# Optimization experiments

Measured on AMD Instinct MI355X. Metric: run time of the kernel, lower is better.

The kernel has to match this reference:

```python
import jax, jax.numpy as jnp
import numpy as np

SMU_ALPHA = 0.25
SMU_MU = 1.0e6  # repo's act.SMU default: large mu -> smooth leaky-relu (max(x, alpha*x))

def smu(x):
    a = SMU_ALPHA
    return 0.5 * ((1.0 + a) * x + (1.0 - a) * x * jax.lax.erf(SMU_MU * (1.0 - a) * x))

def setup_inputs() -> dict:
    key = jax.random.key(0)
    ks = jax.random.split(key, 6)
    B, N, D = 8, 4096, 1024
    xavier = float(np.sqrt(6.0 / (D + D)))
    def lin_w(k):
        return jax.random.uniform(k, (D, D), jnp.float32, -xavier, xavier)
    return {
        "x": jax.random.normal(ks[0], (B, N, D), jnp.float32),
        "Wvr": lin_w(ks[1]), "bvr": jnp.zeros((D,), jnp.float32),
        "Wvi": lin_w(ks[2]), "bvi": jnp.zeros((D,), jnp.float32),
        "Wk": lin_w(ks[3]), "bk": jnp.zeros((D,), jnp.float32),
        "Wq": lin_w(ks[4]), "bq": jnp.zeros((D,), jnp.float32),
    }

def reference(x, Wvr, bvr, Wvi, bvi, Wk, bk, Wq, bq):
    # real input: real and imag branches both see x
    value_real = jnp.einsum('bnd,ed->bne', x, Wvr) + bvr
    value_imag = jnp.einsum('bnd,ed->bne', x, Wvi) + bvi
    # GLU: v_real * tanh(softplus(v_imag)); dropout disabled (p=0)
    value = value_real * jnp.tanh(jax.nn.softplus(value_imag))
    key_ = jnp.einsum('bnd,ed->bne', x, Wk) + bk
    query = jnp.einsum('bnd,ed->bne', x, Wq) + bq
    # L2 normalize along the sequence dim (dim=1)
    key_n = key_ / (jnp.linalg.norm(key_, axis=1, keepdims=True) + 1e-5)
    query_n = query / (jnp.linalg.norm(query, axis=1, keepdims=True) + 1e-5)
    feature_attn = smu(jnp.einsum('bnd,bne->bde', key_n, query_n))  # [B, D, D]
    return jnp.einsum('bnd,bde->bne', value, feature_attn)
```

## Files before the change

### kernel.cpp

```cpp
#include <hip/hip_runtime.h>
#include <math.h>

typedef __bf16 bf16x8 __attribute__((ext_vector_type(8)));
typedef float f32x4 __attribute__((ext_vector_type(4)));

#define MTOT 32768
#define DD   1024
#define NSEQ 4096
#define BB   8

__device__ __forceinline__ void async16(const void* gp, void* lp) {
  __builtin_amdgcn_global_load_lds(
      (__attribute__((address_space(1))) void*)(const_cast<void*>(gp)),
      (__attribute__((address_space(3))) void*)(lp), 16, 0, 0);
}

__device__ __forceinline__ unsigned short f2bf(float f) {
  union { float f; unsigned int u; } v; v.f = f;
  unsigned int r = v.u + 0x7fffu + ((v.u >> 16) & 1u);
  return (unsigned short)(r >> 16);
}
__device__ __forceinline__ float bf2f(unsigned short u) {
  union { unsigned int u; float f; } v; v.u = ((unsigned int)u) << 16; return v.f;
}
__device__ __forceinline__ unsigned pk2(float a, float b) {
  return (unsigned)f2bf(a) | ((unsigned)f2bf(b) << 16);
}

__device__ __forceinline__ unsigned lds_off(void* p) {
  return (unsigned)(unsigned long long)
      (__attribute__((address_space(3))) void*)p;
}
#define DSRI(dst, base, off) \
  asm volatile("ds_read_b128 %0, %1 offset:" #off : "=v"(dst) : "v"(base))

#define MFMA_ __builtin_amdgcn_mfma_f32_16x16x32_bf16

__global__ void cvt_bf16(const float* __restrict__ in, unsigned short* __restrict__ out, int n) {
  int i = (blockIdx.x * blockDim.x + threadIdx.x) * 8;
  if (i >= n) return;
  float4 a = *(const float4*)(in + i);
  float4 b = *(const float4*)(in + i + 4);
  ushort4 o0, o1;
  o0.x = f2bf(a.x); o0.y = f2bf(a.y); o0.z = f2bf(a.z); o0.w = f2bf(a.w);
  o1.x = f2bf(b.x); o1.y = f2bf(b.y); o1.z = f2bf(b.z); o1.w = f2bf(b.w);
  *(ushort4*)(out + i) = o0;
  *(ushort4*)(out + i + 4) = o1;
}

__global__ void cvt_w(const float* __restrict__ w0, const float* __restrict__ w1,
                      const float* __restrict__ w2, const float* __restrict__ w3,
                      unsigned short* __restrict__ out) {
  int z = blockIdx.y;
  const float* in = (z == 0) ? w0 : (z == 1) ? w1 : (z == 2) ? w2 : w3;
  int i = (blockIdx.x * blockDim.x + threadIdx.x) * 8;
  float4 a = *(const float4*)(in + i);
  float4 b = *(const float4*)(in + i + 4);
  ushort4 o0, o1;
  o0.x = f2bf(a.x); o0.y = f2bf(a.y); o0.z = f2bf(a.z); o0.w = f2bf(a.w);
  o1.x = f2bf(b.x); o1.y = f2bf(b.y); o1.z = f2bf(b.z); o1.w = f2bf(b.w);
  unsigned short* o = out + (size_t)z * DD * DD;
  *(ushort4*)(o + i) = o0;
  *(ushort4*)(o + i + 4) = o1;
}

template<int LDG>
__device__ __forceinline__ void stage_half(const unsigned short* __restrict__ g,
                                           int row0, int k0,
                                           unsigned short* lds, int tid) {
#pragma unroll
  for (int l = 0; l < 2; ++l) {
    int u = l * 512 + tid;
    int r = u >> 3;
    int sl = (u & 7) ^ (r & 7);
    async16(g + (size_t)(row0 + r) * LDG + k0 + sl * 8, (char*)lds + u * 16);
  }
}

__global__ __launch_bounds__(512, 2) void proj_all(
    const unsigned short* __restrict__ xb,
    const unsigned short* __restrict__ Wb,
    const float* __restrict__ bvr, const float* __restrict__ bvi,
    const float* __restrict__ bk,  const float* __restrict__ bq,
    unsigned short* __restrict__ oV,
    unsigned short* __restrict__ Kt,  unsigned short* __restrict__ Qt,
    float* __restrict__ rnacc) {
  __shared__ __align__(16) unsigned short smem[65536];

  const int bx = blockIdx.x;
  const int swz = (bx & 7) * 64 + (bx >> 3);
  const int m0 = (swz >> 2) * 256;
  const int n0 = (swz & 3) * 256;
  const int z = blockIdx.z;

  const int tid = threadIdx.x;
  const int w = tid >> 6, lane = tid & 63;
  const int wr = w >> 2, wc = w & 3;
  const int lq = lane >> 4, lr = lane & 15;
  const int sx = lr & 7;
  const int arow0 = wr * 128 + lr;
  const int brow0 = wc * 64 + lr;

  f32x4 acc[8][4];
#pragma unroll
  for (int i = 0; i < 8; i++)
#pragma unroll
    for (int j = 0; j < 4; j++) acc[i][j] = (f32x4)(0.f);

  unsigned pkx[8][4], pky[8][4];

  const int NT = 16;

  const unsigned sbase = lds_off(smem);
  const unsigned sw0 = (unsigned)((lq ^ sx) << 4);
  const unsigned sw1 = (unsigned)(((4 | lq) ^ sx) << 4);
  unsigned aA0 = sbase + arow0 * 128 + sw0;
  unsigned aA1 = sbase + arow0 * 128 + sw1;
  unsigned aB0 = sbase + 32768 + brow0 * 128 + sw0;
  unsigned aB1 = sbase + 32768 + brow0 * 128 + sw1;

  const int npass = (z == 0) ? 2 : 1;
  for (int pass = 0; pass < npass; ++pass) {
    const unsigned short* W =
        (z == 0) ? (Wb + (size_t)(pass == 0 ? 1 : 0) * DD * DD)
                 : (Wb + (size_t)(z + 1) * DD * DD);

    stage_half<1024>(xb, m0,       0,  smem,                     tid);
    stage_half<1024>(xb, m0 + 128, 0,  smem + 8192,              tid);
    stage_half<1024>(W,  n0,       0,  smem + 16384,             tid);
    stage_half<1024>(W,  n0 + 128, 0,  smem + 16384 + 8192,      tid);
    stage_half<1024>(W,  n0,       64, smem + 32768 + 16384,     tid);
    stage_half<1024>(W,  n0 + 128, 64, smem + 32768 + 16384 + 8192, tid);
    asm volatile("s_waitcnt vmcnt(4)" ::: "memory");
    __builtin_amdgcn_s_barrier();

    for (int t = 0; t < NT; ++t) {
      bf16x8 bfr[4][2], aL[4][2];
      DSRI(aL[0][0], aA0, 0);    DSRI(aL[0][1], aA1, 0);
      DSRI(bfr[0][0], aB0, 0);    DSRI(bfr[0][1], aB1, 0);
      DSRI(bfr[1][0], aB0, 2048); DSRI(bfr[1][1], aB1, 2048);
      DSRI(bfr[2][0], aB0, 4096); DSRI(bfr[2][1], aB1, 4096);
      DSRI(bfr[3][0], aB0, 6144); DSRI(bfr[3][1], aB1, 6144);
      DSRI(aL[1][0], aA0, 2048); DSRI(aL[1][1], aA1, 2048);
      DSRI(aL[2][0], aA0, 4096); DSRI(aL[2][1], aA1, 4096);
      DSRI(aL[3][0], aA0, 6144); DSRI(aL[3][1], aA1, 6144);
      if (t + 1 < NT) {
        stage_half<1024>(xb, m0,       (t + 1) * 64, smem + ((t + 1) & 1) * 32768, tid);
        stage_half<1024>(xb, m0 + 128, (t + 1) * 64, smem + ((t + 1) & 1) * 32768 + 8192, tid);
      }
      __builtin_amdgcn_s_barrier();
      asm volatile("s_waitcnt lgkmcnt(6)" ::: "memory");
      __builtin_amdgcn_sched_barrier(0);
      __builtin_amdgcn_s_setprio(1);
#pragma unroll
      for (int nj = 0; nj < 4; ++nj) {
        acc[0][nj] = MFMA_(aL[0][0], bfr[nj][0], acc[0][nj], 0, 0, 0);
        acc[0][nj] = MFMA_(aL[0][1], bfr[nj][1], acc[0][nj], 0, 0, 0);
      }
      asm volatile("s_waitcnt lgkmcnt(0)" ::: "memory");
      __builtin_amdgcn_sched_barrier(0);
#pragma unroll
      for (int mi = 1; mi < 4; ++mi)
#pragma unroll
        for (int nj = 0; nj < 4; ++nj) {
          acc[mi][nj] = MFMA_(aL[mi][0], bfr[nj][0], acc[mi][nj], 0, 0, 0);
          acc[mi][nj] = MFMA_(aL[mi][1], bfr[nj][1], acc[mi][nj], 0, 0, 0);
        }
      __builtin_amdgcn_s_setprio(0);
      __builtin_amdgcn_sched_barrier(0);
      __builtin_amdgcn_s_barrier();

      bf16x8 aH[4][2];
      DSRI(aH[0][0], aA0, 8192);  DSRI(aH[0][1], aA1, 8192);
      DSRI(aH[1][0], aA0, 10240); DSRI(aH[1][1], aA1, 10240);
      DSRI(aH[2][0], aA0, 12288); DSRI(aH[2][1], aA1, 12288);
      DSRI(aH[3][0], aA0, 14336); DSRI(aH[3][1], aA1, 14336);
      if (t + 2 < NT) {
        stage_half<1024>(W, n0,       (t + 2) * 64, smem + (t & 1) * 32768 + 16384, tid);
        stage_half<1024>(W, n0 + 128, (t + 2) * 64, smem + (t & 1) * 32768 + 16384 + 8192, tid);
      }
      __builtin_amdgcn_s_barrier();
      asm volatile("s_waitcnt lgkmcnt(4)" ::: "memory");
      __builtin_amdgcn_sched_barrier(0);
      __builtin_amdgcn_s_setprio(1);
#pragma unroll
      for (int mi = 0; mi < 2; ++mi)
#pragma unroll
        for (int nj = 0; nj < 4; ++nj) {
          acc[4 + mi][nj] = MFMA_(aH[mi][0], bfr[nj][0], acc[4 + mi][nj], 0, 0, 0);
          acc[4 + mi][nj] = MFMA_(aH[mi][1], bfr[nj][1], acc[4 + mi][nj], 0, 0, 0);
        }
      asm volatile("s_waitcnt lgkmcnt(0)" ::: "memory");
      __builtin_amdgcn_sched_barrier(0);
#pragma unroll
      for (int mi = 2; mi < 4; ++mi)
#pragma unroll
        for (int nj = 0; nj < 4; ++nj) {
          acc[4 + mi][nj] = MFMA_(aH[mi][0], bfr[nj][0], acc[4 + mi][nj], 0, 0, 0);
          acc[4 + mi][nj] = MFMA_(aH[mi][1], bfr[nj][1], acc[4 + mi][nj], 0, 0, 0);
        }
      __builtin_amdgcn_s_setprio(0);
      __builtin_amdgcn_sched_barrier(0);
      if (t < NT - 2)       asm volatile("s_waitcnt vmcnt(4)" ::: "memory");
      else if (t == NT - 2) asm volatile("s_waitcnt vmcnt(0)" ::: "memory");
      __builtin_amdgcn_s_barrier();

      aA0 ^= 65536u; aA1 ^= 65536u; aB0 ^= 65536u; aB1 ^= 65536u;
    }

    if (z == 0 && pass == 0) {
#pragma unroll
      for (int nj = 0; nj < 4; ++nj) {
        int col = n0 + wc * 64 + nj * 16 + lr;
        float bv = bvi[col];
#pragma unroll
        for (int mrep = 0; mrep < 8; ++mrep) {
          pkx[mrep][nj] = pk2(acc[mrep][nj][0] + bv, acc[mrep][nj][1] + bv);
          pky[mrep][nj] = pk2(acc[mrep][nj][2] + bv, acc[mrep][nj][3] + bv);
          acc[mrep][nj] = (f32x4)(0.f);
        }
      }
    }
  }

  if (z == 0) {
#pragma unroll
    for (int nj = 0; nj < 4; ++nj) {
      int col = n0 + wc * 64 + nj * 16 + lr;
      float bv = bvr[col];
#pragma unroll
      for (int mrep = 0; mrep < 8; ++mrep) {
        int rowb = m0 + wr * 128 + mrep * 16 + lq * 4;
#pragma unroll
        for (int r = 0; r < 4; ++r) {
          float vr = bf2f(f2bf(acc[mrep][nj][r] + bv));
          unsigned p = (r < 2) ? pkx[mrep][nj] : pky[mrep][nj];
          float vi = bf2f((unsigned short)((r & 1) ? (p >> 16) : (p & 0xffffu)));
          float g;
          if (vi > 10.f) g = 1.f;
          else { float tt = __expf(vi); float u = tt * (tt + 2.f); g = u / (u + 2.f); }
          oV[(size_t)(rowb + r) * DD + col] = f2bf(vr * g);
        }
      }
    }
  } else {
    const float* bias = (z == 1) ? bk : bq;
    unsigned short* outp = (z == 1) ? Kt : Qt;
    const int which = z - 1;
    const int b = m0 >> 12;
    const int nbase = m0 & 4095;
    float* racc = rnacc + which * (BB * DD) + b * DD;
    unsigned short* T = smem;
    const int SP2 = 264;
#pragma unroll
    for (int ch = 0; ch < 2; ++ch) {
      if ((wc >> 1) == ch) {
#pragma unroll
        for (int nj = 0; nj < 4; ++nj) {
          int cloc = (wc & 1) * 64 + nj * 16 + lr;
          float bv = bias[n0 + ch * 128 + cloc];
#pragma unroll
          for (int mrep = 0; mrep < 8; ++mrep) {
            int rowb = wr * 128 + mrep * 16 + lq * 4;
            ushort4 pk;
            pk.x = f2bf(acc[mrep][nj][0] + bv); pk.y = f2bf(acc[mrep][nj][1] + bv);
            pk.z = f2bf(acc[mrep][nj][2] + bv); pk.w = f2bf(acc[mrep][nj][3] + bv);
            *(ushort4*)(T + cloc * SP2 + rowb) = pk;
          }
        }
      }
      __syncthreads();
#pragma unroll
      for (int p = 0; p < 8; ++p) {
        int dl = p * 16 + (tid >> 5);
        int nc = (tid & 31) * 8;
        ushort4 v0 = *(const ushort4*)(T + dl * SP2 + nc);
        ushort4 v1 = *(const ushort4*)(T + dl * SP2 + nc + 4);
        int d = n0 + ch * 128 + dl;
        *(ushort4*)(outp + (size_t)(b * DD + d) * NSEQ + nbase + nc)     = v0;
        *(ushort4*)(outp + (size_t)(b * DD + d) * NSEQ + nbase + nc + 4) = v1;
        float s = bf2f(v0.x)*bf2f(v0.x) + bf2f(v0.y)*bf2f(v0.y) + bf2f(v0.z)*bf2f(v0.z) + bf2f(v0.w)*bf2f(v0.w)
                + bf2f(v1.x)*bf2f(v1.x) + bf2f(v1.y)*bf2f(v1.y) + bf2f(v1.z)*bf2f(v1.z) + bf2f(v1.w)*bf2f(v1.w);
#pragma unroll
        for (int off = 1; off < 32; off <<= 1) s += __shfl_xor(s, off, 32);
        if ((tid & 31) == 0) atomicAdd(&racc[d], s);
      }
      __syncthreads();
    }
  }
}

__global__ void finalize_rn(float* __restrict__ rn) {
  int i = blockIdx.x * blockDim.x + threadIdx.x;
  rn[i] = 1.f / (sqrtf(rn[i]) + 1e-5f);
}

__global__ __launch_bounds__(512, 2) void attn_gemm(
    const unsigned short* __restrict__ Qt, const unsigned short* __restrict__ Kt,
    const float* __restrict__ rn, unsigned short* __restrict__ fat) {
  __shared__ __align__(16) unsigned short smem[57344];

  const int b = blockIdx.z;
  const int d0 = blockIdx.x * 128;
  const int e0 = blockIdx.y * 256;
  const unsigned short* A  = Qt + (size_t)b * DD * NSEQ;
  const unsigned short* Bm = Kt + (size_t)b * DD * NSEQ;
  unsigned short* out = fat + (size_t)b * DD * DD;

  const int tid = threadIdx.x;
  const int w = tid >> 6, lane = tid & 63;
  const int wr = w >> 1, wc = w & 1;
  const int lq = lane >> 4, lr = lane & 15;
  const int sx = lr & 7;
  const int arow0 = wr * 64 + lr;
  const int brow0 = wc * 64 + lr;

  f32x4 acc[4][4];
#pragma unroll
  for (int i = 0; i < 4; i++)
#pragma unroll
    for (int j = 0; j < 4; j++) acc[i][j] = (f32x4)(0.f);

  const int NT = 64;

  const unsigned sbase = lds_off(smem);
  const unsigned sw0 = (unsigned)((lq ^ sx) << 4);
  const unsigned sw1 = (unsigned)(((4 | lq) ^ sx) << 4);
  unsigned aA0 = sbase + arow0 * 128 + sw0;
  unsigned aA1 = sbase + arow0 * 128 + sw1;
  unsigned aB0 = sbase + 32768 + brow0 * 128 + sw0;
  unsigned aB1 = sbase + 32768 + brow0 * 128 + sw1;

  stage_half<NSEQ>(A,  e0,       0,  smem,                 tid);
  stage_half<NSEQ>(A,  e0 + 128, 0,  smem + 8192,          tid);
  stage_half<NSEQ>(Bm, d0,       0,  smem + 16384,         tid);
  stage_half<NSEQ>(Bm, d0,       64, smem + 32768 + 16384, tid);
  asm volatile("s_waitcnt vmcnt(2)" ::: "memory");
  __builtin_amdgcn_s_barrier();

  for (int t = 0; t < NT; ++t) {
    bf16x8 bfr[4][2], aL[2][2];
    DSRI(aL[0][0], aA0, 0);    DSRI(aL[0][1], aA1, 0);
    DSRI(bfr[0][0], aB0, 0);    DSRI(bfr[0][1], aB1, 0);
    DSRI(bfr[1][0], aB0, 2048); DSRI(bfr[1][1], aB1, 2048);
    DSRI(bfr[2][0], aB0, 4096); DSRI(bfr[2][1], aB1, 4096);
    DSRI(bfr[3][0], aB0, 6144); DSRI(bfr[3][1], aB1, 6144);
    DSRI(aL[1][0], aA0, 2048); DSRI(aL[1][1], aA1, 2048);
    if (t + 1 < NT) {
      stage_half<NSEQ>(A, e0,       (t + 1) * 64, smem + ((t + 1) & 1) * 32768, tid);
      stage_half<NSEQ>(A, e0 + 128, (t + 1) * 64, smem + ((t + 1) & 1) * 32768 + 8192, tid);
    }
    __builtin_amdgcn_s_barrier();
    asm volatile("s_waitcnt lgkmcnt(2)" ::: "memory");
    __builtin_amdgcn_sched_barrier(0);
    __builtin_amdgcn_s_setprio(1);
#pragma unroll
    for (int nj = 0; nj < 4; ++nj) {
      acc[0][nj] = MFMA_(aL[0][0], bfr[nj][0], acc[0][nj], 0, 0, 0);
      acc[0][nj] = MFMA_(aL[0][1], bfr[nj][1], acc[0][nj], 0, 0, 0);
    }
    asm volatile("s_waitcnt lgkmcnt(0)" ::: "memory");
    __builtin_amdgcn_sched_barrier(0);
#pragma unroll
    for (int nj = 0; nj < 4; ++nj) {
      acc[1][nj] = MFMA_(aL[1][0], bfr[nj][0], acc[1][nj], 0, 0, 0);
      acc[1][nj] = MFMA_(aL[1][1], bfr[nj][1], acc[1][nj], 0, 0, 0);
    }
    __builtin_amdgcn_s_setprio(0);
    __builtin_amdgcn_sched_barrier(0);
    __builtin_amdgcn_s_barrier();

    bf16x8 aH[2][2];
    DSRI(aH[0][0], aA0, 4096); DSRI(aH[0][1], aA1, 4096);
    DSRI(aH[1][0], aA0, 6144); DSRI(aH[1][1], aA1, 6144);
    if (t + 2 < NT) {
      stage_half<NSEQ>(Bm, d0, (t + 2) * 64, smem + (t & 1) * 32768 + 16384, tid);
    }
    __builtin_amdgcn_s_barrier();
    asm volatile("s_waitcnt lgkmcnt(2)" ::: "memory");
    __builtin_amdgcn_sched_barrier(0);
    __builtin_amdgcn_s_setprio(1);
#pragma unroll
    for (int nj = 0; nj < 4; ++nj) {
      acc[2][nj] = MFMA_(aH[0][0], bfr[nj][0], acc[2][nj], 0, 0, 0);
      acc[2][nj] = MFMA_(aH[0][1], bfr[nj][1], acc[2][nj], 0, 0, 0);
    }
    asm volatile("s_waitcnt lgkmcnt(0)" ::: "memory");
    __builtin_amdgcn_sched_barrier(0);
#pragma unroll
    for (int nj = 0; nj < 4; ++nj) {
      acc[3][nj] = MFMA_(aH[1][0], bfr[nj][0], acc[3][nj], 0, 0, 0);
      acc[3][nj] = MFMA_(aH[1][1], bfr[nj][1], acc[3][nj], 0, 0, 0);
    }
    __builtin_amdgcn_s_setprio(0);
    __builtin_amdgcn_sched_barrier(0);
    if (t < NT - 2)       asm volatile("s_waitcnt vmcnt(2)" ::: "memory");
    else if (t == NT - 2) asm volatile("s_waitcnt vmcnt(0)" ::: "memory");
    __builtin_amdgcn_s_barrier();

    aA0 ^= 65536u; aA1 ^= 65536u; aB0 ^= 65536u; aB1 ^= 65536u;
  }

#pragma unroll
  for (int nj = 0; nj < 4; ++nj) {
    int col = d0 + wc * 64 + nj * 16 + lr;
    float rk = rn[b * DD + col];
#pragma unroll
    for (int mi = 0; mi < 4; ++mi) {
      int rowb = e0 + wr * 64 + mi * 16 + lq * 4;
#pragma unroll
      for (int r = 0; r < 4; ++r) {
        float rq = rn[BB * DD + b * DD + rowb + r];
        float c = acc[mi][nj][r] * rq * rk;
        c = (c > 0.f) ? c : 0.25f * c;
        out[(size_t)(rowb + r) * DD + col] = f2bf(c);
      }
    }
  }
}

__global__ __launch_bounds__(512, 2) void out_gemm(
    const unsigned short* __restrict__ V, const unsigned short* __restrict__ fat,
    float* __restrict__ out) {
  __shared__ __align__(16) unsigned short smem[65536];

  const int bx = blockIdx.x;
  const int swz = (bx & 7) * 64 + (bx >> 3);
  const int m0 = (swz >> 2) * 256;
  const int e0 = (swz & 3) * 256;
  const int b = m0 >> 12;
  const unsigned short* Bm = fat + (size_t)b * DD * DD;

  const int tid = threadIdx.x;
  const int w = tid >> 6, lane = tid & 63;
  const int wr = w >> 2, wc = w & 3;
  const int lq = lane >> 4, lr = lane & 15;
  const int sx = lr & 7;
  const int arow0 = wr * 128 + lr;
  const int brow0 = wc * 64 + lr;

  f32x4 acc[8][4];
#pragma unroll
  for (int i = 0; i < 8; i++)
#pragma unroll
    for (int j = 0; j < 4; j++) acc[i][j] = (f32x4)(0.f);

  const int NT = 16;

  const unsigned sbase = lds_off(smem);
  const unsigned sw0 = (unsigned)((lq ^ sx) << 4);
  const unsigned sw1 = (unsigned)(((4 | lq) ^ sx) << 4);
  unsigned aA0 = sbase + arow0 * 128 + sw0;
  unsigned aA1 = sbase + arow0 * 128 + sw1;
  unsigned aB0 = sbase + 32768 + brow0 * 128 + sw0;
  unsigned aB1 = sbase + 32768 + brow0 * 128 + sw1;

  stage_half<1024>(V,  m0,       0,  smem,                        tid);
  stage_half<1024>(V,  m0 + 128, 0,  smem + 8192,                 tid);
  stage_half<1024>(Bm, e0,       0,  smem + 16384,                tid);
  stage_half<1024>(Bm, e0 + 128, 0,  smem + 16384 + 8192,         tid);
  stage_half<1024>(Bm, e0,       64, smem + 32768 + 16384,        tid);
  stage_half<1024>(Bm, e0 + 128, 64, smem + 32768 + 16384 + 8192, tid);
  asm volatile("s_waitcnt vmcnt(4)" ::: "memory");
  __builtin_amdgcn_s_barrier();

  for (int t = 0; t < NT; ++t) {
    bf16x8 bfr[4][2], aL[4][2];
    DSRI(aL[0][0], aA0, 0);    DSRI(aL[0][1], aA1, 0);
    DSRI(bfr[0][0], aB0, 0);    DSRI(bfr[0][1], aB1, 0);
    DSRI(bfr[1][0], aB0, 2048); DSRI(bfr[1][1], aB1, 2048);
    DSRI(bfr[2][0], aB0, 4096); DSRI(bfr[2][1], aB1, 4096);
    DSRI(bfr[3][0], aB0, 6144); DSRI(bfr[3][1], aB1, 6144);
    DSRI(aL[1][0], aA0, 2048); DSRI(aL[1][1], aA1, 2048);
    DSRI(aL[2][0], aA0, 4096); DSRI(aL[2][1], aA1, 4096);
    DSRI(aL[3][0], aA0, 6144); DSRI(aL[3][1], aA1, 6144);
    if (t + 1 < NT) {
      stage_half<1024>(V, m0,       (t + 1) * 64, smem + ((t + 1) & 1) * 32768, tid);
      stage_half<1024>(V, m0 + 128, (t + 1) * 64, smem + ((t + 1) & 1) * 32768 + 8192, tid);
    }
    __builtin_amdgcn_s_barrier();
    asm volatile("s_waitcnt lgkmcnt(6)" ::: "memory");
    __builtin_amdgcn_sched_barrier(0);
    __builtin_amdgcn_s_setprio(1);
#pragma unroll
    for (int nj = 0; nj < 4; ++nj) {
      acc[0][nj] = MFMA_(aL[0][0], bfr[nj][0], acc[0][nj], 0, 0, 0);
      acc[0][nj] = MFMA_(aL[0][1], bfr[nj][1], acc[0][nj], 0, 0, 0);
    }
    asm volatile("s_waitcnt lgkmcnt(0)" ::: "memory");
    __builtin_amdgcn_sched_barrier(0);
#pragma unroll
    for (int mi = 1; mi < 4; ++mi)
#pragma unroll
      for (int nj = 0; nj < 4; ++nj) {
        acc[mi][nj] = MFMA_(aL[mi][0], bfr[nj][0], acc[mi][nj], 0, 0, 0);
        acc[mi][nj] = MFMA_(aL[mi][1], bfr[nj][1], acc[mi][nj], 0, 0, 0);
      }
    __builtin_amdgcn_s_setprio(0);
    __builtin_amdgcn_sched_barrier(0);
    __builtin_amdgcn_s_barrier();

    bf16x8 aH[4][2];
    DSRI(aH[0][0], aA0, 8192);  DSRI(aH[0][1], aA1, 8192);
    DSRI(aH[1][0], aA0, 10240); DSRI(aH[1][1], aA1, 10240);
    DSRI(aH[2][0], aA0, 12288); DSRI(aH[2][1], aA1, 12288);
    DSRI(aH[3][0], aA0, 14336); DSRI(aH[3][1], aA1, 14336);
    if (t + 2 < NT) {
      stage_half<1024>(Bm, e0,       (t + 2) * 64, smem + (t & 1) * 32768 + 16384, tid);
      stage_half<1024>(Bm, e0 + 128, (t + 2) * 64, smem + (t & 1) * 32768 + 16384 + 8192, tid);
    }
    __builtin_amdgcn_s_barrier();
    asm volatile("s_waitcnt lgkmcnt(4)" ::: "memory");
    __builtin_amdgcn_sched_barrier(0);
    __builtin_amdgcn_s_setprio(1);
#pragma unroll
    for (int mi = 0; mi < 2; ++mi)
#pragma unroll
      for (int nj = 0; nj < 4; ++nj) {
        acc[4 + mi][nj] = MFMA_(aH[mi][0], bfr[nj][0], acc[4 + mi][nj], 0, 0, 0);
        acc[4 + mi][nj] = MFMA_(aH[mi][1], bfr[nj][1], acc[4 + mi][nj], 0, 0, 0);
      }
    asm volatile("s_waitcnt lgkmcnt(0)" ::: "memory");
    __builtin_amdgcn_sched_barrier(0);
#pragma unroll
    for (int mi = 2; mi < 4; ++mi)
#pragma unroll
      for (int nj = 0; nj < 4; ++nj) {
        acc[4 + mi][nj] = MFMA_(aH[mi][0], bfr[nj][0], acc[4 + mi][nj], 0, 0, 0);
        acc[4 + mi][nj] = MFMA_(aH[mi][1], bfr[nj][1], acc[4 + mi][nj], 0, 0, 0);
      }
    __builtin_amdgcn_s_setprio(0);
    __builtin_amdgcn_sched_barrier(0);
    if (t < NT - 2)       asm volatile("s_waitcnt vmcnt(4)" ::: "memory");
    else if (t == NT - 2) asm volatile("s_waitcnt vmcnt(0)" ::: "memory");
    __builtin_amdgcn_s_barrier();

    aA0 ^= 65536u; aA1 ^= 65536u; aB0 ^= 65536u; aB1 ^= 65536u;
  }

#pragma unroll
  for (int nj = 0; nj < 4; ++nj) {
    int col = e0 + wc * 64 + nj * 16 + lr;
#pragma unroll
    for (int mrep = 0; mrep < 8; ++mrep) {
      int rowb = m0 + wr * 128 + mrep * 16 + lq * 4;
#pragma unroll
      for (int r = 0; r < 4; ++r)
        out[(size_t)(rowb + r) * DD + col] = acc[mrep][nj][r];
    }
  }
}

extern "C" void kernel_launch(void* const* d_in, const int* in_sizes, int n_in,
                              void* d_out, int out_size, void* d_ws, size_t ws_size,
                              hipStream_t stream) {
  const float* x   = (const float*)d_in[0];
  const float* Wvr = (const float*)d_in[1];
  const float* bvr = (const float*)d_in[2];
  const float* Wvi = (const float*)d_in[3];
  const float* bvi = (const float*)d_in[4];
  const float* Wk  = (const float*)d_in[5];
  const float* bk  = (const float*)d_in[6];
  const float* Wq  = (const float*)d_in[7];
  const float* bq  = (const float*)d_in[8];
  float* out = (float*)d_out;

  char* p = (char*)d_ws;
  unsigned short* xb  = (unsigned short*)p; p += (size_t)MTOT * DD * 2;
  unsigned short* Wb  = (unsigned short*)p; p += 4ull * DD * DD * 2;
  unsigned short* Kt  = (unsigned short*)p; p += (size_t)BB * DD * NSEQ * 2;
  unsigned short* Qt  = (unsigned short*)p; p += (size_t)BB * DD * NSEQ * 2;
  unsigned short* Vb  = (unsigned short*)p; p += (size_t)MTOT * DD * 2;
  unsigned short* fat = (unsigned short*)p; p += (size_t)BB * DD * DD * 2;
  float* rn = (float*)p; p += 2ull * BB * DD * sizeof(float);

  int nx = MTOT * DD;
  int nw = DD * DD;
  cvt_bf16<<<nx / 8 / 256, 256, 0, stream>>>(x, xb, nx);
  cvt_w<<<dim3(nw / 8 / 256, 4), 256, 0, stream>>>(Wvr, Wvi, Wk, Wq, Wb);
  hipMemsetAsync(rn, 0, 2ull * BB * DD * sizeof(float), stream);

  proj_all<<<dim3(512, 1, 3), 512, 0, stream>>>(
      xb, Wb, bvr, bvi, bk, bq, Vb, Kt, Qt, rn);

  finalize_rn<<<2 * BB * DD / 256, 256, 0, stream>>>(rn);

  attn_gemm<<<dim3(DD / 128, DD / 256, BB), 512, 0, stream>>>(Qt, Kt, rn, fat);
  out_gemm<<<dim3(512), 512, 0, stream>>>(Vb, fat, out);
}
```

Before: 717.0 us.

## Split value projection into dedicated kernel computing real and imag GEMMs together

The fused projection kernel had z=0 blocks running two sequential GEMM passes (imag then real), which made them twice as long as the K/Q blocks and unbalanced the grid. A new proj_v kernel uses 256x128 tiles and computes both Wvr and Wvi products at once from a shared x tile, so each x load feeds two GEMMs. K/Q projection becomes its own kernel with the same tiling as before. This balances work across blocks and halves x traffic for the value branch. The cost is an extra launch, a smaller N tile per block, and more accumulator registers.

```diff
diff --git a/kernel.cpp b/kernel.cpp
--- a/kernel.cpp
+++ b/kernel.cpp
@@ -22,9 +22,6 @@
 }
 __device__ __forceinline__ float bf2f(unsigned short u) {
   union { unsigned int u; float f; } v; v.u = ((unsigned int)u) << 16; return v.f;
-}
-__device__ __forceinline__ unsigned pk2(float a, float b) {
-  return (unsigned)f2bf(a) | ((unsigned)f2bf(b) << 16);
 }
 
 __device__ __forceinline__ unsigned lds_off(void* p) {
@@ -77,12 +74,140 @@
   }
 }
 
-__global__ __launch_bounds__(512, 2) void proj_all(
+__global__ __launch_bounds__(512, 2) void proj_v(
     const unsigned short* __restrict__ xb,
     const unsigned short* __restrict__ Wb,
     const float* __restrict__ bvr, const float* __restrict__ bvi,
+    unsigned short* __restrict__ oV) {
+  __shared__ __align__(16) unsigned short smem[65536];
+
+  const int bx = blockIdx.x;
+  const int swz = (bx & 7) * 128 + (bx >> 3);
+  const int m0 = (swz >> 3) * 256;
+  const int n0 = (swz & 7) * 128;
+  const unsigned short* Wr = Wb;
+  const unsigned short* Wi = Wb + (size_t)DD * DD;
+
+  const int tid = threadIdx.x;
+  const int w = tid >> 6, lane = tid & 63;
+  const int wrow = w >> 1, wcol = w & 1;
+  const int lq = lane >> 4, lr = lane & 15;
+  const int sx = lr & 7;
+  const int arow0 = wrow * 64 + lr;
+  const int brow0 = wcol * 64 + lr;
+
+  f32x4 accr[4][4], acci[4][4];
+#pragma unroll
+  for (int i = 0; i < 4; i++)
+#pragma unroll
+    for (int j = 0; j < 4; j++) { accr[i][j] = (f32x4)(0.f); acci[i][j] = (f32x4)(0.f); }
+
+  const int NT = 16;
+
+  const unsigned sbase = lds_off(smem);
+  const unsigned sw0 = (unsigned)((lq ^ sx) << 4);
+  const unsigned sw1 = (unsigned)(((4 | lq) ^ sx) << 4);
+  unsigned aA0 = sbase + arow0 * 128 + sw0;
+  unsigned aA1 = sbase + arow0 * 128 + sw1;
+  unsigned aR0 = sbase + 32768 + brow0 * 128 + sw0;
+  unsigned aR1 = sbase + 32768 + brow0 * 128 + sw1;
+  unsigned aI0 = sbase + 49152 + brow0 * 128 + sw0;
+  unsigned aI1 = sbase + 49152 + brow0 * 128 + sw1;
+
+  stage_half<1024>(xb, m0,       0,  smem,                  tid);
+  stage_half<1024>(xb, m0 + 128, 0,  smem + 8192,           tid);
+  stage_half<1024>(Wr, n0,       0,  smem + 16384,          tid);
+  stage_half<1024>(Wi, n0,       0,  smem + 24576,          tid);
+  stage_half<1024>(Wr, n0,       64, smem + 32768 + 16384,  tid);
+  stage_half<1024>(Wi, n0,       64, smem + 32768 + 24576,  tid);
+  asm volatile("s_waitcnt vmcnt(4)" ::: "memory");
+  __builtin_amdgcn_s_barrier();
+
+  for (int t = 0; t < NT; ++t) {
+    bf16x8 aF[4][2], bR[4][2], bI[4][2];
+    DSRI(aF[0][0], aA0, 0);    DSRI(aF[0][1], aA1, 0);
+    DSRI(bR[0][0], aR0, 0);    DSRI(bR[0][1], aR1, 0);
+    DSRI(bR[1][0], aR0, 2048); DSRI(bR[1][1], aR1, 2048);
+    DSRI(bR[2][0], aR0, 4096); DSRI(bR[2][1], aR1, 4096);
+    DSRI(bR[3][0], aR0, 6144); DSRI(bR[3][1], aR1, 6144);
+    DSRI(aF[1][0], aA0, 2048); DSRI(aF[1][1], aA1, 2048);
+    DSRI(aF[2][0], aA0, 4096); DSRI(aF[2][1], aA1, 4096);
+    DSRI(aF[3][0], aA0, 6144); DSRI(aF[3][1], aA1, 6144);
+    DSRI(bI[0][0], aI0, 0);    DSRI(bI[0][1], aI1, 0);
+    DSRI(bI[1][0], aI0, 2048); DSRI(bI[1][1], aI1, 2048);
+    DSRI(bI[2][0], aI0, 4096); DSRI(bI[2][1], aI1, 4096);
+    DSRI(bI[3][0], aI0, 6144); DSRI(bI[3][1], aI1, 6144);
+    if (t + 1 < NT) {
+      stage_half<1024>(xb, m0,       (t + 1) * 64, smem + ((t + 1) & 1) * 32768, tid);
+      stage_half<1024>(xb, m0 + 128, (t + 1) * 64, smem + ((t + 1) & 1) * 32768 + 8192, tid);
+    }
+    asm volatile("s_waitcnt lgkmcnt(14)" ::: "memory");
+    __builtin_amdgcn_sched_barrier(0);
+    __builtin_amdgcn_s_setprio(1);
+#pragma unroll
+    for (int nj = 0; nj < 4; ++nj) {
+      accr[0][nj] = MFMA_(aF[0][0], bR[nj][0], accr[0][nj], 0, 0, 0);
+      accr[0][nj] = MFMA_(aF[0][1], bR[nj][1], accr[0][nj], 0, 0, 0);
+    }
+    asm volatile("s_waitcnt lgkmcnt(8)" ::: "memory");
+    __builtin_amdgcn_sched_barrier(0);
+#pragma unroll
+    for (int mi = 1; mi < 4; ++mi)
+#pragma unroll
+      for (int nj = 0; nj < 4; ++nj) {
+        accr[mi][nj] = MFMA_(aF[mi][0], bR[nj][0], accr[mi][nj], 0, 0, 0);
+        accr[mi][nj] = MFMA_(aF[mi][1], bR[nj][1], accr[mi][nj], 0, 0, 0);
+      }
+    __builtin_amdgcn_s_setprio(0);
+    asm volatile("s_waitcnt lgkmcnt(0)" ::: "memory");
+    __builtin_amdgcn_sched_barrier(0);
+    __builtin_amdgcn_s_barrier();
+    if (t + 2 < NT) {
+      stage_half<1024>(Wr, n0, (t + 2) * 64, smem + (t & 1) * 32768 + 16384, tid);
+      stage_half<1024>(Wi, n0, (t + 2) * 64, smem + (t & 1) * 32768 + 24576, tid);
+    }
+    __builtin_amdgcn_s_setprio(1);
+#pragma unroll
+    for (int mi = 0; mi < 4; ++mi)
+#pragma unroll
+      for (int nj = 0; nj < 4; ++nj) {
+        acci[mi][nj] = MFMA_(aF[mi][0], bI[nj][0], acci[mi][nj], 0, 0, 0);
+        acci[mi][nj] = MFMA_(aF[mi][1], bI[nj][1], acci[mi][nj], 0, 0, 0);
+      }
+    __builtin_amdgcn_s_setprio(0);
+    __builtin_amdgcn_sched_barrier(0);
+    if (t < NT - 2)       asm volatile("s_waitcnt vmcnt(4)" ::: "memory");
+    else if (t == NT - 2) asm volatile("s_waitcnt vmcnt(0)" ::: "memory");
+    __builtin_amdgcn_s_barrier();
+
+    aA0 ^= 65536u; aA1 ^= 65536u; aR0 ^= 65536u; aR1 ^= 65536u;
+    aI0 ^= 65536u; aI1 ^= 65536u;
+  }
+
+#pragma unroll
+  for (int nj = 0; nj < 4; ++nj) {
+    int col = n0 + wcol * 64 + nj * 16 + lr;
+    float br_ = bvr[col], bi_ = bvi[col];
+#pragma unroll
+    for (int mi = 0; mi < 4; ++mi) {
+      int rowb = m0 + wrow * 64 + mi * 16 + lq * 4;
+#pragma unroll
+      for (int r = 0; r < 4; ++r) {
+        float vr = bf2f(f2bf(accr[mi][nj][r] + br_));
+        float vi = bf2f(f2bf(acci[mi][nj][r] + bi_));
+        float g;
+        if (vi > 10.f) g = 1.f;
+        else { float tt = __expf(vi); float u = tt * (tt + 2.f); g = u / (u + 2.f); }
+        oV[(size_t)(rowb + r) * DD + col] = f2bf(vr * g);
+      }
+    }
+  }
+}
+
+__global__ __launch_bounds__(512, 2) void proj_kq(
+    const unsigned short* __restrict__ xb,
+    const unsigned short* __restrict__ Wb,
     const float* __restrict__ bk,  const float* __restrict__ bq,
-    unsigned short* __restrict__ oV,
     unsigned short* __restrict__ Kt,  unsigned short* __restrict__ Qt,
     float* __restrict__ rnacc) {
   __shared__ __align__(16) unsigned short smem[65536];
@@ -92,6 +217,8 @@
   const int m0 = (swz >> 2) * 256;
   const int n0 = (swz & 3) * 256;
   const int z = blockIdx.z;
+  const unsigned short* W = Wb + (size_t)(2 + z) * DD * DD;
+  const float* bias = (z == 0) ? bk : bq;
 
   const int tid = threadIdx.x;
   const int w = tid >> 6, lane = tid & 63;
@@ -107,8 +234,6 @@
 #pragma unroll
     for (int j = 0; j < 4; j++) acc[i][j] = (f32x4)(0.f);
 
-  unsigned pkx[8][4], pky[8][4];
-
   const int NT = 16;
 
   const unsigned sbase = lds_off(smem);
@@ -119,137 +244,94 @@
   unsigned aB0 = sbase + 32768 + brow0 * 128 + sw0;
   unsigned aB1 = sbase + 32768 + brow0 * 128 + sw1;
 
-  const int npass = (z == 0) ? 2 : 1;
-  for (int pass = 0; pass < npass; ++pass) {
-    const unsigned short* W =
-        (z == 0) ? (Wb + (size_t)(pass == 0 ? 1 : 0) * DD * DD)
-                 : (Wb + (size_t)(z + 1) * DD * DD);
-
-    stage_half<1024>(xb, m0,       0,  smem,                     tid);
-    stage_half<1024>(xb, m0 + 128, 0,  smem + 8192,              tid);
-    stage_half<1024>(W,  n0,       0,  smem + 16384,             tid);
-    stage_half<1024>(W,  n0 + 128, 0,  smem + 16384 + 8192,      tid);
-    stage_half<1024>(W,  n0,       64, smem + 32768 + 16384,     tid);
-    stage_half<1024>(W,  n0 + 128, 64, smem + 32768 + 16384 + 8192, tid);
-    asm volatile("s_waitcnt vmcnt(4)" ::: "memory");
-    __builtin_amdgcn_s_barrier();
-
-    for (int t = 0; t < NT; ++t) {
-      bf16x8 bfr[4][2], aL[4][2];
-      DSRI(aL[0][0], aA0, 0);    DSRI(aL[0][1], aA1, 0);
-      DSRI(bfr[0][0], aB0, 0);    DSRI(bfr[0][1], aB1, 0);
-      DSRI(bfr[1][0], aB0, 2048); DSRI(bfr[1][1], aB1, 2048);
-      DSRI(bfr[2][0], aB0, 4096); DSRI(bfr[2][1], aB1, 4096);
-      DSRI(bfr[3][0], aB0, 6144); DSRI(bfr[3][1], aB1, 6144);
-      DSRI(aL[1][0], aA0, 2048); DSRI(aL[1][1], aA1, 2048);
-      DSRI(aL[2][0], aA0, 4096); DSRI(aL[2][1], aA1, 4096);
-      DSRI(aL[3][0], aA0, 6144); DSRI(aL[3][1], aA1, 6144);
-      if (t + 1 < NT) {
-        stage_half<1024>(xb, m0,       (t + 1) * 64, smem + ((t + 1) & 1) * 32768, tid);
-        stage_half<1024>(xb, m0 + 128, (t + 1) * 64, smem + ((t + 1) & 1) * 32768 + 8192, tid);
-      }
-      __builtin_amdgcn_s_barrier();
-      asm volatile("s_waitcnt lgkmcnt(6)" ::: "memory");
-      __builtin_amdgcn_sched_barrier(0);
-      __builtin_amdgcn_s_setprio(1);
-#pragma unroll
-      for (int nj = 0; nj < 4; ++nj) {
-        acc[0][nj] = MFMA_(aL[0][0], bfr[nj][0], acc[0][nj], 0, 0, 0);
-        acc[0][nj] = MFMA_(aL[0][1], bfr[nj][1], acc[0][nj], 0, 0, 0);
-      }
-      asm volatile("s_waitcnt lgkmcnt(0)" ::: "memory");
-      __builtin_amdgcn_sched_barrier(0);
-#pragma unroll
-      for (int mi = 1; mi < 4; ++mi)
-#pragma unroll
-        for (int nj = 0; nj < 4; ++nj) {
-          acc[mi][nj] = MFMA_(aL[mi][0], bfr[nj][0], acc[mi][nj], 0, 0, 0);
-          acc[mi][nj] = MFMA_(aL[mi][1], bfr[nj][1], acc[mi][nj], 0, 0, 0);
-        }
-      __builtin_amdgcn_s_setprio(0);
-      __builtin_amdgcn_sched_barrier(0);
-      __builtin_amdgcn_s_barrier();
-
-      bf16x8 aH[4][2];
-      DSRI(aH[0][0], aA0, 8192);  DSRI(aH[0][1], aA1, 8192);
-      DSRI(aH[1][0], aA0, 10240); DSRI(aH[1][1], aA1, 10240);
-      DSRI(aH[2][0], aA0, 12288); DSRI(aH[2][1], aA1, 12288);
-      DSRI(aH[3][0], aA0, 14336); DSRI(aH[3][1], aA1, 14336);
-      if (t + 2 < NT) {
-        stage_half<1024>(W, n0,       (t + 2) * 64, smem + (t & 1) * 32768 + 16384, tid);
-        stage_half<1024>(W, n0 + 128, (t + 2) * 64, smem + (t & 1) * 32768 + 16384 + 8192, tid);
-      }
-      __builtin_amdgcn_s_barrier();
-      asm volatile("s_waitcnt lgkmcnt(4)" ::: "memory");
-      __builtin_amdgcn_sched_barrier(0);
-      __builtin_amdgcn_s_setprio(1);
-#pragma unroll
-      for (int mi = 0; mi < 2; ++mi)
-#pragma unroll
-        for (int nj = 0; nj < 4; ++nj) {
-          acc[4 + mi][nj] = MFMA_(aH[mi][0], bfr[nj][0], acc[4 + mi][nj], 0, 0, 0);
-          acc[4 + mi][nj] = MFMA_(aH[mi][1], bfr[nj][1], acc[4 + mi][nj], 0, 0, 0);
-        }
-      asm volatile("s_waitcnt lgkmcnt(0)" ::: "memory");
-      __builtin_amdgcn_sched_barrier(0);
-#pragma unroll
-      for (int mi = 2; mi < 4; ++mi)
-#pragma unroll
-        for (int nj = 0; nj < 4; ++nj) {
-          acc[4 + mi][nj] = MFMA_(aH[mi][0], bfr[nj][0], acc[4 + mi][nj], 0, 0, 0);
-          acc[4 + mi][nj] = MFMA_(aH[mi][1], bfr[nj][1], acc[4 + mi][nj], 0, 0, 0);
-        }
-      __builtin_amdgcn_s_setprio(0);
-      __builtin_amdgcn_sched_barrier(0);
-      if (t < NT - 2)       asm volatile("s_waitcnt vmcnt(4)" ::: "memory");
-      else if (t == NT - 2) asm volatile("s_waitcnt vmcnt(0)" ::: "memory");
-      __builtin_amdgcn_s_barrier();
-
-      aA0 ^= 65536u; aA1 ^= 65536u; aB0 ^= 65536u; aB1 ^= 65536u;
-    }
-
-    if (z == 0 && pass == 0) {
-#pragma unroll
-      for (int nj = 0; nj < 4; ++nj) {
-        int col = n0 + wc * 64 + nj * 16 + lr;
-        float bv = bvi[col];
-#pragma unroll
-        for (int mrep = 0; mrep < 8; ++mrep) {
-          pkx[mrep][nj] = pk2(acc[mrep][nj][0] + bv, acc[mrep][nj][1] + bv);
-          pky[mrep][nj] = pk2(acc[mrep][nj][2] + bv, acc[mrep][nj][3] + bv);
-          acc[mrep][nj] = (f32x4)(0.f);
-        }
-      }
-    }
-  }
-
-  if (z == 0) {
+  stage_half<1024>(xb, m0,       0,  smem,                     tid);
+  stage_half<1024>(xb, m0 + 128, 0,  smem + 8192,              tid);
+  stage_half<1024>(W,  n0,       0,  smem + 16384,             tid);
+  stage_half<1024>(W,  n0 + 128, 0,  smem + 16384 + 8192,      tid);
+  stage_half<1024>(W,  n0,       64, smem + 32768 + 16384,     tid);
+  stage_half<1024>(W,  n0 + 128, 64, smem + 32768 + 16384 + 8192, tid);
+  asm volatile("s_waitcnt vmcnt(4)" ::: "memory");
+  __builtin_amdgcn_s_barrier();
+
+  for (int t = 0; t < NT; ++t) {
+    bf16x8 bfr[4][2], aL[4][2];
+    DSRI(aL[0][0], aA0, 0);    DSRI(aL[0][1], aA1, 0);
+    DSRI(bfr[0][0], aB0, 0);    DSRI(bfr[0][1], aB1, 0);
+    DSRI(bfr[1][0], aB0, 2048); DSRI(bfr[1][1], aB1, 2048);
+    DSRI(bfr[2][0], aB0, 4096); DSRI(bfr[2][1], aB1, 4096);
+    DSRI(bfr[3][0], aB0, 6144); DSRI(bfr[3][1], aB1, 6144);
+    DSRI(aL[1][0], aA0, 2048); DSRI(aL[1][1], aA1, 2048);
+    DSRI(aL[2][0], aA0, 4096); DSRI(aL[2][1], aA1, 4096);
+    DSRI(aL[3][0], aA0, 6144); DSRI(aL[3][1], aA1, 6144);
+    if (t + 1 < NT) {
+      stage_half<1024>(xb, m0,       (t + 1) * 64, smem + ((t + 1) & 1) * 32768, tid);
+      stage_half<1024>(xb, m0 + 128, (t + 1) * 64, smem + ((t + 1) & 1) * 32768 + 8192, tid);
+    }
+    __builtin_amdgcn_s_barrier();
+    asm volatile("s_waitcnt lgkmcnt(6)" ::: "memory");
+    __builtin_amdgcn_sched_barrier(0);
+    __builtin_amdgcn_s_setprio(1);
 #pragma unroll
     for (int nj = 0; nj < 4; ++nj) {
-      int col = n0 + wc * 64 + nj * 16 + lr;
-      float bv = bvr[col];
-#pragma unroll
-      for (int mrep = 0; mrep < 8; ++mrep) {
-        int rowb = m0 + wr * 128 + mrep * 16 + lq * 4;
-#pragma unroll
-        for (int r = 0; r < 4; ++r) {
-          float vr = bf2f(f2bf(acc[mrep][nj][r] + bv));
-          unsigned p = (r < 2) ? pkx[mrep][nj] : pky[mrep][nj];
-          float vi = bf2f((unsigned short)((r & 1) ? (p >> 16) : (p & 0xffffu)));
-          float g;
-          if (vi > 10.f) g = 1.f;
-          else { float tt = __expf(vi); float u = tt * (tt + 2.f); g = u / (u + 2.f); }
-          oV[(size_t)(rowb + r) * DD + col] = f2bf(vr * g);
-        }
-      }
-    }
-  } else {
-    const float* bias = (z == 1) ? bk : bq;
-    unsigned short* outp = (z == 1) ? Kt : Qt;
-    const int which = z - 1;
+      acc[0][nj] = MFMA_(aL[0][0], bfr[nj][0], acc[0][nj], 0, 0, 0);
+      acc[0][nj] = MFMA_(aL[0][1], bfr[nj][1], acc[0][nj], 0, 0, 0);
+    }
+    asm volatile("s_waitcnt lgkmcnt(0)" ::: "memory");
+    __builtin_amdgcn_sched_barrier(0);
+#pragma unroll
+    for (int mi = 1; mi < 4; ++mi)
+#pragma unroll
+      for (int nj = 0; nj < 4; ++nj) {
+        acc[mi][nj] = MFMA_(aL[mi][0], bfr[nj][0], acc[mi][nj], 0, 0, 0);
+        acc[mi][nj] = MFMA_(aL[mi][1], bfr[nj][1], acc[mi][nj], 0, 0, 0);
+      }
+    __builtin_amdgcn_s_setprio(0);
+    __builtin_amdgcn_sched_barrier(0);
+    __builtin_amdgcn_s_barrier();
+
+    bf16x8 aH[4][2];
+    DSRI(aH[0][0], aA0, 8192);  DSRI(aH[0][1], aA1, 8192);
+    DSRI(aH[1][0], aA0, 10240); DSRI(aH[1][1], aA1, 10240);
+    DSRI(aH[2][0], aA0, 12288); DSRI(aH[2][1], aA1, 12288);
+    DSRI(aH[3][0], aA0, 14336); DSRI(aH[3][1], aA1, 14336);
+    if (t + 2 < NT) {
+      stage_half<1024>(W, n0,       (t + 2) * 64, smem + (t & 1) * 32768 + 16384, tid);
+      stage_half<1024>(W, n0 + 128, (t + 2) * 64, smem + (t & 1) * 32768 + 16384 + 8192, tid);
+    }
+    __builtin_amdgcn_s_barrier();
+    asm volatile("s_waitcnt lgkmcnt(4)" ::: "memory");
+    __builtin_amdgcn_sched_barrier(0);
+    __builtin_amdgcn_s_setprio(1);
+#pragma unroll
+    for (int mi = 0; mi < 2; ++mi)
+#pragma unroll
+      for (int nj = 0; nj < 4; ++nj) {
+        acc[4 + mi][nj] = MFMA_(aH[mi][0], bfr[nj][0], acc[4 + mi][nj], 0, 0, 0);
+        acc[4 + mi][nj] = MFMA_(aH[mi][1], bfr[nj][1], acc[4 + mi][nj], 0, 0, 0);
+      }
+    asm volatile("s_waitcnt lgkmcnt(0)" ::: "memory");
+    __builtin_amdgcn_sched_barrier(0);
+#pragma unroll
+    for (int mi = 2; mi < 4; ++mi)
+#pragma unroll
+      for (int nj = 0; nj < 4; ++nj) {
+        acc[4 + mi][nj] = MFMA_(aH[mi][0], bfr[nj][0], acc[4 + mi][nj], 0, 0, 0);
+        acc[4 + mi][nj] = MFMA_(aH[mi][1], bfr[nj][1], acc[4 + mi][nj], 0, 0, 0);
+      }
+    __builtin_amdgcn_s_setprio(0);
+    __builtin_amdgcn_sched_barrier(0);
+    if (t < NT - 2)       asm volatile("s_waitcnt vmcnt(4)" ::: "memory");
+    else if (t == NT - 2) asm volatile("s_waitcnt vmcnt(0)" ::: "memory");
+    __builtin_amdgcn_s_barrier();
+
+    aA0 ^= 65536u; aA1 ^= 65536u; aB0 ^= 65536u; aB1 ^= 65536u;
+  }
+
+  {
+    unsigned short* outp = (z == 0) ? Kt : Qt;
     const int b = m0 >> 12;
     const int nbase = m0 & 4095;
-    float* racc = rnacc + which * (BB * DD) + b * DD;
+    float* racc = rnacc + z * (BB * DD) + b * DD;
     unsigned short* T = smem;
     const int SP2 = 264;
 #pragma unroll
@@ -580,8 +662,8 @@
   cvt_w<<<dim3(nw / 8 / 256, 4), 256, 0, stream>>>(Wvr, Wvi, Wk, Wq, Wb);
   hipMemsetAsync(rn, 0, 2ull * BB * DD * sizeof(float), stream);
 
-  proj_all<<<dim3(512, 1, 3), 512, 0, stream>>>(
-      xb, Wb, bvr, bvi, bk, bq, Vb, Kt, Qt, rn);
+  proj_v<<<dim3(1024), 512, 0, stream>>>(xb, Wb, bvr, bvi, Vb);
+  proj_kq<<<dim3(512, 1, 2), 512, 0, stream>>>(xb, Wb, bk, bq, Kt, Qt, rn);
 
   finalize_rn<<<2 * BB * DD / 256, 256, 0, stream>>>(rn);
 
```

Measured after the change: 723.4 us. No clear change (+0.9%).
